# Performance work log

Measured on AMD Instinct MI355X. Metric: run time of the kernel, lower is better.

The kernel has to match this reference:

```python
import jax, jax.numpy as jnp
import numpy as np

EPS = 1e-5
GAMMA = 1.0


def _conv(x, w, b):
    # x: NCHW, w: OIHW, stride 1, padding 1 ('SAME' for 3x3)
    y = jax.lax.conv_general_dilated(x, w, (1, 1), 'SAME',
                                     dimension_numbers=('NCHW', 'OIHW', 'NCHW'))
    return y + b[None, :, None, None]


def _maxpool2(x):
    return jax.lax.reduce_window(x, -jnp.inf, jax.lax.max,
                                 (1, 1, 2, 2), (1, 1, 2, 2), 'VALID')


def setup_inputs() -> dict:
    key = jax.random.key(0)
    ks = jax.random.split(key, 24)
    f32 = jnp.float32
    d = {}
    d['x'] = jax.random.normal(ks[0], (8192, 1, 28, 28), dtype=f32)
    d['conv1_w'] = jax.random.normal(ks[1], (8, 1, 3, 3), dtype=f32) * 0.1
    d['conv1_b'] = jax.random.normal(ks[2], (8,), dtype=f32) * 0.1
    d['conv2_w'] = jax.random.normal(ks[3], (16, 8, 3, 3), dtype=f32) * 0.1
    d['conv2_b'] = jax.random.normal(ks[4], (16,), dtype=f32) * 0.1
    d['fc1_w'] = jax.random.normal(ks[5], (64, 784), dtype=f32) * 0.03
    d['fc1_b'] = jax.random.normal(ks[6], (64,), dtype=f32) * 0.03
    d['fc2_w'] = jax.random.normal(ks[7], (4, 64), dtype=f32) * 0.1
    d['fc2_b'] = jax.random.normal(ks[8], (4,), dtype=f32) * 0.1
    d['bn_g'] = jnp.ones((4,), dtype=f32)
    d['bn_b'] = jnp.zeros((4,), dtype=f32)
    d['samp_w1'] = jax.random.normal(ks[9], (4, 2), dtype=f32) * 0.5
    d['samp_b1'] = jax.random.normal(ks[10], (4,), dtype=f32) * 0.1
    d['samp_w2'] = jax.random.normal(ks[11], (2, 4), dtype=f32) * 0.5
    d['samp_b2'] = jax.random.normal(ks[12], (2,), dtype=f32) * 0.1
    d['est_w1'] = jax.random.normal(ks[13], (8, 2), dtype=f32) * 0.5
    d['est_b1'] = jax.random.normal(ks[14], (8,), dtype=f32) * 0.1
    d['est_w2'] = jax.random.normal(ks[15], (4, 8), dtype=f32) * 0.5
    d['est_b2'] = jax.random.normal(ks[16], (4,), dtype=f32) * 0.1
    d['est_w3'] = jax.random.normal(ks[17], (1, 4), dtype=f32) * 0.5
    d['est_b3'] = jax.random.normal(ks[18], (1,), dtype=f32) * 0.1
    d['memory'] = jax.random.normal(ks[19], (10, 4), dtype=f32)
    return d


def reference(x, conv1_w, conv1_b, conv2_w, conv2_b,
              fc1_w, fc1_b, fc2_w, fc2_b, bn_g, bn_b,
              samp_w1, samp_b1, samp_w2, samp_b2,
              est_w1, est_b1, est_w2, est_b2, est_w3, est_b3,
              memory):
    bsz = x.shape[0]
    # CNN features
    h = _maxpool2(jax.nn.relu(_conv(x, conv1_w, conv1_b)))          # (B,8,14,14)
    h = _maxpool2(jax.nn.relu(_conv(h, conv2_w, conv2_b)))          # (B,16,7,7)
    flat = h.reshape(bsz, -1)                                       # (B,784)
    # FC head + BatchNorm1d (training-mode batch stats, biased var)
    fc = jax.nn.relu(flat @ fc1_w.T + fc1_b) @ fc2_w.T + fc2_b      # (B,4)
    mu = jnp.mean(fc, axis=0)
    var = jnp.var(fc, axis=0)
    logits = bn_g * (fc - mu) / jnp.sqrt(var + EPS) + bn_b
    # Sampler on first 2 flat features
    s = jnp.tanh(flat[:, :2] @ samp_w1.T + samp_b1) @ samp_w2.T + samp_b2
    sample_probs = jax.nn.softmax(s, axis=-1)
    # Estimator (EstimatorNN expects 2 input features)
    e = jnp.tanh(flat[:, :2] @ est_w1.T + est_b1)
    e = jnp.tanh(e @ est_w2.T + est_b2)
    regression_output = e @ est_w3.T + est_b3                       # (B,1)
    # Vectorized RBF Gram matrix between flat[:, :4] and memory (10,4)
    q = flat[:, :4]
    sq = jnp.sum(q * q, axis=1, keepdims=True) \
         + jnp.sum(memory * memory, axis=1)[None, :] \
         - 2.0 * (q @ memory.T)
    kernel_matrix = jnp.exp(-GAMMA * sq)                            # (B,10)
    return (logits, sample_probs, regression_output, kernel_matrix)
```

## Files before the change

kernel.cpp:

```cpp
#include <hip/hip_runtime.h>
#include <math.h>

#define EPS_BN 1e-5f

typedef float  f32x4  __attribute__((ext_vector_type(4)));
typedef float  f32x2  __attribute__((ext_vector_type(2)));
typedef short  bf16x8 __attribute__((ext_vector_type(8)));

__device__ inline unsigned short f2bf(float f) {
    union { float f; unsigned u; } c; c.f = f;
    unsigned u = c.u;
    return (unsigned short)((u + 0x7FFFu + ((u >> 16) & 1u)) >> 16);
}

__global__ __launch_bounds__(256, 8) void k_conv(
    const float* __restrict__ x,
    const float* __restrict__ c1w, const float* __restrict__ c1b,
    const float* __restrict__ c2w, const float* __restrict__ c2b,
    const float* __restrict__ fc1w, unsigned short* __restrict__ Bp,
    unsigned short* __restrict__ flatb, float* __restrict__ exact4g, int bsz)
{
    __shared__ float sx[2][900];
    __shared__ __align__(16) unsigned short s1t[2][16][16][8];
    __shared__ float s1f[2][4][12][8];
    __shared__ __align__(16) unsigned short sBc2[1536];
    __shared__ unsigned short lut16[56];

    const int tid  = threadIdx.x;
    const int img0 = blockIdx.x * 2;

    if (blockIdx.x < 200) {
        int t = blockIdx.x * 256 + tid;
        int j  = t & 7;
        int l  = (t >> 3) & 63;
        int nf = (t >> 9) & 3;
        int kb = t >> 11;
        int k  = kb * 32 + (l >> 4) * 8 + j;
        int o  = nf * 16 + (l & 15);
        float v = (k < 784) ? fc1w[o * 784 + k] : 0.f;
        Bp[t] = f2bf(v);
    }

    for (int t = tid; t < 1536; t += 256) {
        int j  = t & 7;
        int l  = (t >> 3) & 63;
        int g  = t >> 9;
        int kp = 4 * g + (l >> 4);
        int oc = l & 15;
        float v = (kp < 9) ? c2w[(oc * 8 + j) * 9 + kp] : 0.f;
        sBc2[t] = f2bf(v);
    }

    if (tid < 52) lut16[tid] = (unsigned short)(256 * (tid / 7) + 16 * (tid % 7));

    if (tid < 232) {
        int im = tid / 116;
        int r  = tid - im * 116;
        int idx;
        if      (r < 30) idx = r;
        else if (r < 60) idx = 29 * 30 + (r - 30);
        else if (r < 88) idx = (r - 60 + 1) * 30;
        else             idx = (r - 88 + 1) * 30 + 29;
        sx[im][idx] = 0.f;
    }
    {
        const float4* xb4 = (const float4*)(x + (size_t)img0 * 784);
        for (int i = tid; i < 392; i += 256) {
            int im  = i / 196;
            int j   = i - im * 196;
            int row = j / 7;
            int c4  = j - row * 7;
            float4 f = xb4[i];
            float* dp = &sx[im][(row + 1) * 30 + c4 * 4 + 1];
            dp[0] = f.x; dp[1] = f.y; dp[2] = f.z; dp[3] = f.w;
        }
    }
    for (int q = tid; q < 120; q += 256) {
        int im = q / 60, r = q - im * 60;
        int Y, X;
        if      (r < 16) { Y = 0;          X = r; }
        else if (r < 32) { Y = 15;         X = r - 16; }
        else if (r < 46) { Y = r - 32 + 1; X = 0; }
        else             { Y = r - 46 + 1; X = 15; }
        *(uint4*)&s1t[im][Y][X][0] = make_uint4(0, 0, 0, 0);
    }
    for (int q = tid; q < 192; q += 256) ((float4*)s1f)[q] = make_float4(0, 0, 0, 0);
    __syncthreads();

    if (tid < 196) {
        int im  = tid / 98;
        int r   = tid - im * 98;
        int py  = r / 7;
        int pxq = r - py * 7;
        const float* sp = &sx[im][(2 * py) * 30 + 4 * pxq];
        f32x2 rp[4][3], sh[4][2];
        #pragma unroll
        for (int wy = 0; wy < 4; ++wy) {
            rp[wy][0] = *(const f32x2*)(sp + wy * 30);
            rp[wy][1] = *(const f32x2*)(sp + wy * 30 + 2);
            rp[wy][2] = *(const f32x2*)(sp + wy * 30 + 4);
            sh[wy][0] = (f32x2){rp[wy][0].y, rp[wy][1].x};
            sh[wy][1] = (f32x2){rp[wy][1].y, rp[wy][2].x};
        }
        unsigned pk0[4] = {0, 0, 0, 0}, pk1[4] = {0, 0, 0, 0};
        const bool sf = (py <= 2) && (pxq <= 4);
        #pragma unroll
        for (int c = 0; c < 8; ++c) {
            const float* wp = &c1w[c * 9];
            float bb = c1b[c];
            f32x2 A[2][2];
            A[0][0] = (f32x2){bb, bb}; A[0][1] = (f32x2){bb, bb};
            A[1][0] = (f32x2){bb, bb}; A[1][1] = (f32x2){bb, bb};
            #pragma unroll
            for (int ky = 0; ky < 3; ++ky) {
                #pragma unroll
                for (int kx = 0; kx < 3; ++kx) {
                    float wv = wp[ky * 3 + kx];
                    f32x2 wv2 = (f32x2){wv, wv};
                    #pragma unroll
                    for (int dy = 0; dy < 2; ++dy) {
                        int row = dy + ky;
                        f32x2 s0 = (kx == 0) ? rp[row][0] : (kx == 1) ? sh[row][0] : rp[row][1];
                        f32x2 s1v = (kx == 0) ? rp[row][1] : (kx == 1) ? sh[row][1] : rp[row][2];
                        A[0][dy] = __builtin_elementwise_fma(s0,  wv2, A[0][dy]);
                        A[1][dy] = __builtin_elementwise_fma(s1v, wv2, A[1][dy]);
                    }
                }
            }
            f32x2 m0 = __builtin_elementwise_max(A[0][0], A[0][1]);
            f32x2 m1 = __builtin_elementwise_max(A[1][0], A[1][1]);
            float v0 = fmaxf(fmaxf(m0.x, m0.y), 0.f);
            float v1 = fmaxf(fmaxf(m1.x, m1.y), 0.f);
            pk0[c >> 1] |= (unsigned)f2bf(v0) << ((c & 1) * 16);
            pk1[c >> 1] |= (unsigned)f2bf(v1) << ((c & 1) * 16);
            if (sf) {
                s1f[im][py + 1][2 * pxq + 1][c] = v0;
                s1f[im][py + 1][2 * pxq + 2][c] = v1;
            }
        }
        *(uint4*)&s1t[im][py + 1][2 * pxq + 1][0] = make_uint4(pk0[0], pk0[1], pk0[2], pk0[3]);
        *(uint4*)&s1t[im][py + 1][2 * pxq + 2][0] = make_uint4(pk1[0], pk1[1], pk1[2], pk1[3]);
    }
    __syncthreads();

    {
        const int wv   = __builtin_amdgcn_readfirstlane(tid >> 6);
        const int im   = wv >> 1;
        const int half = wv & 1;
        const int l    = tid & 63;
        const int grp  = l >> 4;
        const int m15  = l & 15;

        bf16x8 bfr[3];
        #pragma unroll
        for (int g = 0; g < 3; ++g)
            bfr[g] = *(const bf16x8*)(sBc2 + (size_t)(g * 64 + l) * 8);

        int koff[3];
        #pragma unroll
        for (int g = 0; g < 3; ++g) {
            int kp = 4 * g + grp;
            koff[g] = (kp < 9) ? ((kp / 3) * 16 + (kp % 3)) * 8 : 0;
        }
        const float bias = c2b[m15];
        unsigned short* s2b = (unsigned short*)&sx[im][0];

        const int n   = 7 - half;
        const int qa0 = 4 * half + (m15 >> 2);
        const int sub = ((m15 & 2) >> 1) * 128 + (m15 & 1) * 8;
        const unsigned short* s1b = &s1t[im][0][0][0];

        unsigned roff[7];
        #pragma unroll
        for (int i = 0; i < 7; ++i) {
            if (i < n) {
                int qa = qa0 + 8 * i;
                if (qa > 48) qa = 48;
                roff[i] = lut16[qa];
            }
        }

        int qo = 4 * half + grp;
        #pragma unroll
        for (int i = 0; i < 7; ++i) {
            if (i < n) {
                const unsigned short* ab = s1b + roff[i] + sub;
                f32x4 acc = {};
                #pragma unroll
                for (int g = 0; g < 3; ++g) {
                    bf16x8 a = *(const bf16x8*)(ab + koff[g]);
                    acc = __builtin_amdgcn_mfma_f32_16x16x32_bf16(a, bfr[g], acc, 0, 0, 0);
                }
                float m = fmaxf(fmaxf(acc[0], acc[1]), fmaxf(acc[2], acc[3]));
                float val = fmaxf(m + bias, 0.f);
                if (qo < 49) s2b[m15 * 49 + qo] = f2bf(val);
                qo += 8;
            }
        }

        if (half == 1 && l < 16) {
            int q  = l >> 2;
            int dy = (l >> 1) & 1, dx = l & 1;
            float a = 0.f;
            #pragma unroll
            for (int kp = 0; kp < 9; ++kp) {
                int ky = kp / 3, kx = kp - 3 * ky;
                const float* spf = &s1f[im][dy + ky][2 * q + dx + kx][0];
                #pragma unroll
                for (int ic = 0; ic < 8; ++ic)
                    a += spf[ic] * c2w[ic * 9 + kp];
            }
            float m1 = fmaxf(a, __shfl_xor(a, 1));
            float m2 = fmaxf(m1, __shfl_xor(m1, 2));
            if ((l & 3) == 0)
                exact4g[(size_t)(img0 + im) * 4 + q] = fmaxf(m2 + c2b[0], 0.f);
        }
    }
    __syncthreads();

    if (tid < 200) {
        int im = tid / 100;
        int j  = tid - im * 100;
        const uint4* s2v = (const uint4*)&sx[im][0];
        uint4 v = (j < 98) ? s2v[j] : make_uint4(0, 0, 0, 0);
        *(uint4*)(flatb + (size_t)(img0 + im) * 800 + j * 8) = v;
    }
}

__global__ __launch_bounds__(128) void k_fc(
    const unsigned short* __restrict__ flatb, const unsigned short* __restrict__ Bp,
    const float* __restrict__ fc1b, const float* __restrict__ fc2w,
    const float* __restrict__ fc2b, float* __restrict__ fct,
    float* __restrict__ partial, int bsz)
{
    __shared__ float h[2][16][68];
    __shared__ float ps[2][4][2];

    const int tid  = threadIdx.x;
    const int w    = __builtin_amdgcn_readfirstlane(tid >> 6);
    const int l    = tid & 63;
    const int img0 = blockIdx.x * 32 + w * 16;
    const int m15  = l & 15;
    const int grp  = l >> 4;

    const unsigned short* aptr = flatb + (size_t)(img0 + m15) * 800 + grp * 8;
    const unsigned short* bptr = Bp + (size_t)l * 8;

    f32x4 acc[4] = {};
    for (int kb = 0; kb < 25; ++kb) {
        bf16x8 a = *(const bf16x8*)(aptr + kb * 32);
        #pragma unroll
        for (int nf = 0; nf < 4; ++nf) {
            bf16x8 b = *(const bf16x8*)(bptr + (size_t)(kb * 4 + nf) * 64 * 8);
            acc[nf] = __builtin_amdgcn_mfma_f32_16x16x32_bf16(a, b, acc[nf], 0, 0, 0);
        }
    }

    #pragma unroll
    for (int nf = 0; nf < 4; ++nf) {
        int j = nf * 16 + m15;
        float bj = fc1b[j];
        #pragma unroll
        for (int r = 0; r < 4; ++r)
            h[w][grp * 4 + r][j] = fmaxf(acc[nf][r] + bj, 0.f);
    }
    __syncthreads();

    {
        int im = m15, ch = grp;
        float a = fc2b[ch];
        const float* hp = &h[w][im][0];
        const float* wp = &fc2w[ch * 64];
        #pragma unroll 8
        for (int o = 0; o < 64; ++o) a += hp[o] * wp[o];
        fct[(size_t)ch * bsz + img0 + im] = a;

        float s = a, ss = a * a;
        #pragma unroll
        for (int off = 1; off < 16; off <<= 1) {
            s  += __shfl_xor(s,  off);
            ss += __shfl_xor(ss, off);
        }
        if (m15 == 0) { ps[w][ch][0] = s; ps[w][ch][1] = ss; }
    }
    __syncthreads();

    if (tid < 8) {
        int c = tid & 3, st = tid >> 2;
        partial[(size_t)blockIdx.x * 8 + st * 4 + c] =
            ps[0][c][st] + ps[1][c][st];
    }
}

__global__ __launch_bounds__(256) void k_bnheads(
    const float* __restrict__ partial, const float* __restrict__ g,
    const float* __restrict__ bb, const float* __restrict__ fct,
    const float* __restrict__ exact4g,
    const float* __restrict__ sw1, const float* __restrict__ sb1,
    const float* __restrict__ sw2, const float* __restrict__ sb2,
    const float* __restrict__ ew1, const float* __restrict__ eb1,
    const float* __restrict__ ew2, const float* __restrict__ eb2,
    const float* __restrict__ ew3, const float* __restrict__ eb3,
    const float* __restrict__ mem,
    float* __restrict__ out, int bsz)
{
    __shared__ float red[32][8];
    __shared__ float tot[8];
    __shared__ float sc[4], shf[4];

    const int tid = threadIdx.x;

    {
        int v = tid & 7, chunk = tid >> 3;
        float s = 0.f;
        #pragma unroll
        for (int i = 0; i < 8; ++i)
            s += partial[(size_t)(chunk * 8 + i) * 8 + v];
        red[chunk][v] = s;
    }
    __syncthreads();
    if (tid < 8) {
        float s = 0.f;
        #pragma unroll 8
        for (int c = 0; c < 32; ++c) s += red[c][tid];
        tot[tid] = s;
    }
    __syncthreads();
    if (tid < 4) {
        float n = (float)bsz;
        float mu  = tot[tid] / n;
        float var = tot[4 + tid] / n - mu * mu;
        float scale = g[tid] * rsqrtf(var + EPS_BN);
        sc[tid]  = scale;
        shf[tid] = bb[tid] - mu * scale;
    }
    __syncthreads();

    const int img = blockIdx.x * 256 + tid;
    const int off_samp = bsz * 4;
    const int off_reg  = bsz * 6;
    const int off_ker  = bsz * 7;

    {
        const float4 f = *(const float4*)(exact4g + (size_t)img * 4);
        const float f0 = f.x, f1 = f.y, f2 = f.z, f3 = f.w;
        float qq = f0 * f0 + f1 * f1 + f2 * f2 + f3 * f3;
        #pragma unroll
        for (int j = 0; j < 10; ++j) {
            float m0 = mem[j * 4 + 0], m1 = mem[j * 4 + 1];
            float m2 = mem[j * 4 + 2], m3 = mem[j * 4 + 3];
            float sq = qq + m0 * m0 + m1 * m1 + m2 * m2 + m3 * m3
                     - 2.f * (f0 * m0 + f1 * m1 + f2 * m2 + f3 * m3);
            out[off_ker + (size_t)img * 10 + j] = expf(-sq);
        }
        {
            float t1[4];
            #pragma unroll
            for (int j = 0; j < 4; ++j)
                t1[j] = tanhf(f0 * sw1[j * 2] + f1 * sw1[j * 2 + 1] + sb1[j]);
            float s0 = sb2[0], s1v = sb2[1];
            #pragma unroll
            for (int j = 0; j < 4; ++j) { s0 += t1[j] * sw2[j]; s1v += t1[j] * sw2[4 + j]; }
            float mx = fmaxf(s0, s1v);
            float e0 = expf(s0 - mx), e1 = expf(s1v - mx);
            float inv = 1.f / (e0 + e1);
            out[off_samp + (size_t)img * 2 + 0] = e0 * inv;
            out[off_samp + (size_t)img * 2 + 1] = e1 * inv;
        }
        {
            float e1a[8];
            #pragma unroll
            for (int j = 0; j < 8; ++j)
                e1a[j] = tanhf(f0 * ew1[j * 2] + f1 * ew1[j * 2 + 1] + eb1[j]);
            float rg = eb3[0];
            #pragma unroll
            for (int m = 0; m < 4; ++m) {
                float a = eb2[m];
                #pragma unroll
                for (int j = 0; j < 8; ++j) a += e1a[j] * ew2[m * 8 + j];
                rg += tanhf(a) * ew3[m];
            }
            out[off_reg + img] = rg;
        }
    }

    {
        float4 r;
        r.x = fct[img]           * sc[0] + shf[0];
        r.y = fct[bsz + img]     * sc[1] + shf[1];
        r.z = fct[2 * bsz + img] * sc[2] + shf[2];
        r.w = fct[3 * bsz + img] * sc[3] + shf[3];
        *(float4*)(out + (size_t)img * 4) = r;
    }
}

extern "C" void kernel_launch(void* const* d_in, const int* in_sizes, int n_in,
                              void* d_out, int out_size, void* d_ws, size_t ws_size,
                              hipStream_t stream) {
    const float* x     = (const float*)d_in[0];
    const float* c1w   = (const float*)d_in[1];
    const float* c1b   = (const float*)d_in[2];
    const float* c2w   = (const float*)d_in[3];
    const float* c2b   = (const float*)d_in[4];
    const float* fc1w  = (const float*)d_in[5];
    const float* fc1b  = (const float*)d_in[6];
    const float* fc2w  = (const float*)d_in[7];
    const float* fc2b  = (const float*)d_in[8];
    const float* bng   = (const float*)d_in[9];
    const float* bnb   = (const float*)d_in[10];
    const float* sw1   = (const float*)d_in[11];
    const float* sb1   = (const float*)d_in[12];
    const float* sw2   = (const float*)d_in[13];
    const float* sb2   = (const float*)d_in[14];
    const float* ew1   = (const float*)d_in[15];
    const float* eb1   = (const float*)d_in[16];
    const float* ew2   = (const float*)d_in[17];
    const float* eb2   = (const float*)d_in[18];
    const float* ew3   = (const float*)d_in[19];
    const float* eb3   = (const float*)d_in[20];
    const float* mem   = (const float*)d_in[21];

    const int bsz = in_sizes[0] / 784;
    float* out = (float*)d_out;

    unsigned short* flatb = (unsigned short*)d_ws;
    unsigned short* Bp    = flatb + (size_t)bsz * 800;
    float* fct            = (float*)(Bp + 51200);
    float* partial        = fct + (size_t)bsz * 4;
    float* exact4g        = partial + 2048;

    k_conv<<<bsz / 2, 256, 0, stream>>>(x, c1w, c1b, c2w, c2b,
                                        fc1w, Bp, flatb, exact4g, bsz);
    k_fc<<<bsz / 32, 128, 0, stream>>>(flatb, Bp, fc1b, fc2w, fc2b,
                                       fct, partial, bsz);
    k_bnheads<<<bsz / 256, 256, 0, stream>>>(partial, bng, bnb, fct, exact4g,
                                             sw1, sb1, sw2, sb2,
                                             ew1, eb1, ew2, eb2, ew3, eb3, mem,
                                             out, bsz);
}
```

Measured before the change: 45.69 us.

## Process four images per conv block and use hardware bf16 packing

The fused conv kernel now handles four images per 256-thread block instead of two, halving the grid. Conv2 work is remapped so each wave owns one whole image (13 MFMA tiles) instead of half an image. Conv1 is remapped so each thread produces one pooled pixel per loop iteration, which makes the 784 work items loop unevenly over 256 threads. Software bf16 rounding is replaced with the v_cvt_pk_bf16_f32 instruction. The aim is to amortize per-block setup (weight packing, LUT, padding) over more images and cut conversion instructions, at the cost of more LDS per block and lower occupancy (launch bounds 4).

New measurement: 48.02 us. 5.1% more time.

```diff
diff --git a/kernel.cpp b/kernel.cpp
--- a/kernel.cpp
+++ b/kernel.cpp
@@ -12,22 +12,27 @@
     unsigned u = c.u;
     return (unsigned short)((u + 0x7FFFu + ((u >> 16) & 1u)) >> 16);
 }
-
-__global__ __launch_bounds__(256, 8) void k_conv(
+__device__ inline unsigned cvtpk_bf16(float a, float b) {
+    unsigned r;
+    asm("v_cvt_pk_bf16_f32 %0, %1, %2" : "=v"(r) : "v"(a), "v"(b));
+    return r;
+}
+
+__global__ __launch_bounds__(256, 4) void k_conv(
     const float* __restrict__ x,
     const float* __restrict__ c1w, const float* __restrict__ c1b,
     const float* __restrict__ c2w, const float* __restrict__ c2b,
     const float* __restrict__ fc1w, unsigned short* __restrict__ Bp,
     unsigned short* __restrict__ flatb, float* __restrict__ exact4g, int bsz)
 {
-    __shared__ float sx[2][900];
-    __shared__ __align__(16) unsigned short s1t[2][16][16][8];
-    __shared__ float s1f[2][4][12][8];
+    __shared__ float sx[4][900];
+    __shared__ __align__(16) unsigned short s1t[4][16][16][8];
+    __shared__ float s1f[4][4][12][8];
     __shared__ __align__(16) unsigned short sBc2[1536];
     __shared__ unsigned short lut16[56];
 
     const int tid  = threadIdx.x;
-    const int img0 = blockIdx.x * 2;
+    const int img0 = blockIdx.x * 4;
 
     if (blockIdx.x < 200) {
         int t = blockIdx.x * 256 + tid;
@@ -53,9 +58,9 @@
 
     if (tid < 52) lut16[tid] = (unsigned short)(256 * (tid / 7) + 16 * (tid % 7));
 
-    if (tid < 232) {
-        int im = tid / 116;
-        int r  = tid - im * 116;
+    for (int q = tid; q < 464; q += 256) {
+        int im = q / 116;
+        int r  = q - im * 116;
         int idx;
         if      (r < 30) idx = r;
         else if (r < 60) idx = 29 * 30 + (r - 30);
@@ -65,7 +70,7 @@
     }
     {
         const float4* xb4 = (const float4*)(x + (size_t)img0 * 784);
-        for (int i = tid; i < 392; i += 256) {
+        for (int i = tid; i < 784; i += 256) {
             int im  = i / 196;
             int j   = i - im * 196;
             int row = j / 7;
@@ -75,7 +80,7 @@
             dp[0] = f.x; dp[1] = f.y; dp[2] = f.z; dp[3] = f.w;
         }
     }
-    for (int q = tid; q < 120; q += 256) {
+    for (int q = tid; q < 240; q += 256) {
         int im = q / 60, r = q - im * 60;
         int Y, X;
         if      (r < 16) { Y = 0;          X = r; }
@@ -84,72 +89,59 @@
         else             { Y = r - 46 + 1; X = 15; }
         *(uint4*)&s1t[im][Y][X][0] = make_uint4(0, 0, 0, 0);
     }
-    for (int q = tid; q < 192; q += 256) ((float4*)s1f)[q] = make_float4(0, 0, 0, 0);
-    __syncthreads();
-
-    if (tid < 196) {
-        int im  = tid / 98;
-        int r   = tid - im * 98;
-        int py  = r / 7;
-        int pxq = r - py * 7;
-        const float* sp = &sx[im][(2 * py) * 30 + 4 * pxq];
-        f32x2 rp[4][3], sh[4][2];
+    for (int q = tid; q < 384; q += 256) ((float4*)s1f)[q] = make_float4(0, 0, 0, 0);
+    __syncthreads();
+
+    for (int t = tid; t < 784; t += 256) {
+        int im = t / 196;
+        int r  = t - im * 196;
+        int py = r / 14;
+        int px = r - py * 14;
+        const float* sp = &sx[im][(2 * py) * 30 + 2 * px];
+        f32x2 rp[4][2], shv[4];
         #pragma unroll
         for (int wy = 0; wy < 4; ++wy) {
             rp[wy][0] = *(const f32x2*)(sp + wy * 30);
             rp[wy][1] = *(const f32x2*)(sp + wy * 30 + 2);
-            rp[wy][2] = *(const f32x2*)(sp + wy * 30 + 4);
-            sh[wy][0] = (f32x2){rp[wy][0].y, rp[wy][1].x};
-            sh[wy][1] = (f32x2){rp[wy][1].y, rp[wy][2].x};
-        }
-        unsigned pk0[4] = {0, 0, 0, 0}, pk1[4] = {0, 0, 0, 0};
-        const bool sf = (py <= 2) && (pxq <= 4);
+            shv[wy]   = (f32x2){rp[wy][0].y, rp[wy][1].x};
+        }
+        const bool sf = (py <= 2) && (px <= 10);
+        float v[8];
         #pragma unroll
         for (int c = 0; c < 8; ++c) {
             const float* wp = &c1w[c * 9];
             float bb = c1b[c];
-            f32x2 A[2][2];
-            A[0][0] = (f32x2){bb, bb}; A[0][1] = (f32x2){bb, bb};
-            A[1][0] = (f32x2){bb, bb}; A[1][1] = (f32x2){bb, bb};
+            f32x2 A0 = (f32x2){bb, bb};
+            f32x2 A1 = (f32x2){bb, bb};
             #pragma unroll
             for (int ky = 0; ky < 3; ++ky) {
-                #pragma unroll
-                for (int kx = 0; kx < 3; ++kx) {
-                    float wv = wp[ky * 3 + kx];
-                    f32x2 wv2 = (f32x2){wv, wv};
-                    #pragma unroll
-                    for (int dy = 0; dy < 2; ++dy) {
-                        int row = dy + ky;
-                        f32x2 s0 = (kx == 0) ? rp[row][0] : (kx == 1) ? sh[row][0] : rp[row][1];
-                        f32x2 s1v = (kx == 0) ? rp[row][1] : (kx == 1) ? sh[row][1] : rp[row][2];
-                        A[0][dy] = __builtin_elementwise_fma(s0,  wv2, A[0][dy]);
-                        A[1][dy] = __builtin_elementwise_fma(s1v, wv2, A[1][dy]);
-                    }
-                }
+                float w0 = wp[ky * 3], w1 = wp[ky * 3 + 1], w2 = wp[ky * 3 + 2];
+                f32x2 w0v = (f32x2){w0, w0}, w1v = (f32x2){w1, w1}, w2v = (f32x2){w2, w2};
+                A0 = __builtin_elementwise_fma(rp[ky][0],     w0v, A0);
+                A0 = __builtin_elementwise_fma(shv[ky],       w1v, A0);
+                A0 = __builtin_elementwise_fma(rp[ky][1],     w2v, A0);
+                A1 = __builtin_elementwise_fma(rp[ky + 1][0], w0v, A1);
+                A1 = __builtin_elementwise_fma(shv[ky + 1],   w1v, A1);
+                A1 = __builtin_elementwise_fma(rp[ky + 1][1], w2v, A1);
             }
-            f32x2 m0 = __builtin_elementwise_max(A[0][0], A[0][1]);
-            f32x2 m1 = __builtin_elementwise_max(A[1][0], A[1][1]);
-            float v0 = fmaxf(fmaxf(m0.x, m0.y), 0.f);
-            float v1 = fmaxf(fmaxf(m1.x, m1.y), 0.f);
-            pk0[c >> 1] |= (unsigned)f2bf(v0) << ((c & 1) * 16);
-            pk1[c >> 1] |= (unsigned)f2bf(v1) << ((c & 1) * 16);
-            if (sf) {
-                s1f[im][py + 1][2 * pxq + 1][c] = v0;
-                s1f[im][py + 1][2 * pxq + 2][c] = v1;
-            }
-        }
-        *(uint4*)&s1t[im][py + 1][2 * pxq + 1][0] = make_uint4(pk0[0], pk0[1], pk0[2], pk0[3]);
-        *(uint4*)&s1t[im][py + 1][2 * pxq + 2][0] = make_uint4(pk1[0], pk1[1], pk1[2], pk1[3]);
-    }
-    __syncthreads();
-
-    {
-        const int wv   = __builtin_amdgcn_readfirstlane(tid >> 6);
-        const int im   = wv >> 1;
-        const int half = wv & 1;
-        const int l    = tid & 63;
-        const int grp  = l >> 4;
-        const int m15  = l & 15;
+            f32x2 mx = __builtin_elementwise_max(A0, A1);
+            v[c] = fmaxf(fmaxf(mx.x, mx.y), 0.f);
+            if (sf) s1f[im][py + 1][px + 1][c] = v[c];
+        }
+        uint4 pk;
+        pk.x = cvtpk_bf16(v[0], v[1]);
+        pk.y = cvtpk_bf16(v[2], v[3]);
+        pk.z = cvtpk_bf16(v[4], v[5]);
+        pk.w = cvtpk_bf16(v[6], v[7]);
+        *(uint4*)&s1t[im][py + 1][px + 1][0] = pk;
+    }
+    __syncthreads();
+
+    {
+        const int im  = __builtin_amdgcn_readfirstlane(tid >> 6);
+        const int l   = tid & 63;
+        const int grp = l >> 4;
+        const int m15 = l & 15;
 
         bf16x8 bfr[3];
         #pragma unroll
@@ -164,41 +156,34 @@
         }
         const float bias = c2b[m15];
         unsigned short* s2b = (unsigned short*)&sx[im][0];
-
-        const int n   = 7 - half;
-        const int qa0 = 4 * half + (m15 >> 2);
+        const unsigned short* s1b = &s1t[im][0][0][0];
         const int sub = ((m15 & 2) >> 1) * 128 + (m15 & 1) * 8;
-        const unsigned short* s1b = &s1t[im][0][0][0];
-
-        unsigned roff[7];
-        #pragma unroll
-        for (int i = 0; i < 7; ++i) {
-            if (i < n) {
-                int qa = qa0 + 8 * i;
-                if (qa > 48) qa = 48;
-                roff[i] = lut16[qa];
+
+        unsigned roff[13];
+        #pragma unroll
+        for (int i = 0; i < 13; ++i) {
+            int qa = 4 * i + (m15 >> 2);
+            if (qa > 48) qa = 48;
+            roff[i] = lut16[qa];
+        }
+
+        #pragma unroll
+        for (int i = 0; i < 13; ++i) {
+            const unsigned short* ab = s1b + roff[i] + sub;
+            f32x4 acc = {};
+            #pragma unroll
+            for (int g = 0; g < 3; ++g) {
+                bf16x8 a = *(const bf16x8*)(ab + koff[g]);
+                acc = __builtin_amdgcn_mfma_f32_16x16x32_bf16(a, bfr[g], acc, 0, 0, 0);
             }
-        }
-
-        int qo = 4 * half + grp;
-        #pragma unroll
-        for (int i = 0; i < 7; ++i) {
-            if (i < n) {
-                const unsigned short* ab = s1b + roff[i] + sub;
-                f32x4 acc = {};
-                #pragma unroll
-                for (int g = 0; g < 3; ++g) {
-                    bf16x8 a = *(const bf16x8*)(ab + koff[g]);
-                    acc = __builtin_amdgcn_mfma_f32_16x16x32_bf16(a, bfr[g], acc, 0, 0, 0);
-                }
-                float m = fmaxf(fmaxf(acc[0], acc[1]), fmaxf(acc[2], acc[3]));
-                float val = fmaxf(m + bias, 0.f);
-                if (qo < 49) s2b[m15 * 49 + qo] = f2bf(val);
-                qo += 8;
-            }
-        }
-
-        if (half == 1 && l < 16) {
+            float m = fmaxf(fmaxf(acc[0], acc[1]), fmaxf(acc[2], acc[3]));
+            float val = fmaxf(m + bias, 0.f);
+            int qo = 4 * i + grp;
+            if (qo < 49)
+                s2b[m15 * 49 + qo] = (unsigned short)cvtpk_bf16(val, val);
+        }
+
+        if (l < 16) {
             int q  = l >> 2;
             int dy = (l >> 1) & 1, dx = l & 1;
             float a = 0.f;
@@ -218,9 +203,9 @@
     }
     __syncthreads();
 
-    if (tid < 200) {
-        int im = tid / 100;
-        int j  = tid - im * 100;
+    for (int i = tid; i < 400; i += 256) {
+        int im = i / 100;
+        int j  = i - im * 100;
         const uint4* s2v = (const uint4*)&sx[im][0];
         uint4 v = (j < 98) ? s2v[j] : make_uint4(0, 0, 0, 0);
         *(uint4*)(flatb + (size_t)(img0 + im) * 800 + j * 8) = v;
@@ -429,7 +414,7 @@
     float* partial        = fct + (size_t)bsz * 4;
     float* exact4g        = partial + 2048;
 
-    k_conv<<<bsz / 2, 256, 0, stream>>>(x, c1w, c1b, c2w, c2b,
+    k_conv<<<bsz / 4, 256, 0, stream>>>(x, c1w, c1b, c2w, c2b,
                                         fc1w, Bp, flatb, exact4g, bsz);
     k_fc<<<bsz / 32, 128, 0, stream>>>(flatb, Bp, fc1b, fc2w, fc2b,
                                        fct, partial, bsz);
```
